# Kernel optimization log

Measured on AMD Instinct MI355X. Metric: run time of the kernel, lower is better.

The kernel has to match this reference:

```python
import jax, jax.numpy as jnp
import numpy as np

NHEADS = 16
KVHEADS = 4
HEAD_DIM = 128  # emb_kq_per_head == emb_v_per_head
ROPE_THETA = 10000.0


def _rotary(x, cos, sin):
    # x: [B, S, H, D]; half-split rotation
    x1, x2 = jnp.split(x, 2, axis=-1)
    rot = jnp.concatenate([-x2, x1], axis=-1)
    return x * cos + rot * sin


def setup_inputs() -> dict:
    key = jax.random.key(0)
    k1, k2, k3 = jax.random.split(key, 3)
    B, S, E = 2, 2048, 2048
    qkv_out = NHEADS * HEAD_DIM + 2 * KVHEADS * HEAD_DIM  # 3072
    return {
        "x": jax.random.normal(k1, (B, S, E), dtype=jnp.float32),
        "w_qkv": jax.random.normal(k2, (E, qkv_out), dtype=jnp.float32) * 0.02,
        "w_dense": jax.random.normal(k3, (NHEADS * HEAD_DIM, E), dtype=jnp.float32) * 0.02,
    }


def reference(x, w_qkv, w_dense):
    B, S, E = x.shape
    D = HEAD_DIM
    # fused QKV projection (use_bias=False), then split per FusedQKV.splits
    qkv = x @ w_qkv  # [B, S, 3072]
    q, k, v = jnp.split(qkv, [NHEADS * D, NHEADS * D + KVHEADS * D], axis=-1)
    q = q.reshape(B, S, NHEADS, D)
    k = k.reshape(B, S, KVHEADS, D)
    v = v.reshape(B, S, KVHEADS, D)

    # rotary position encoding, positions = arange(S)
    pos = jnp.arange(S, dtype=jnp.float32)
    inv_freq = 1.0 / (ROPE_THETA ** (jnp.arange(0, D, 2, dtype=jnp.float32) / D))
    ang = pos[:, None] * inv_freq[None, :]                 # [S, D/2]
    ang = jnp.concatenate([ang, ang], axis=-1)             # [S, D]
    cos = jnp.cos(ang)[None, :, None, :]                   # [1, S, 1, D]
    sin = jnp.sin(ang)[None, :, None, :]
    q = _rotary(q, cos, sin)
    k = _rotary(k, cos, sin)

    # GQA: expand kv heads to query heads
    rep = NHEADS // KVHEADS
    k = jnp.repeat(k, rep, axis=2)  # [B, S, NHEADS, D]
    v = jnp.repeat(v, rep, axis=2)

    scale = 1.0 / jnp.sqrt(jnp.asarray(D, dtype=x.dtype))
    scores = jnp.einsum("bqhd,bkhd->bhqk", q, k) * scale   # [B, H, S, S]
    causal = jnp.tril(jnp.ones((S, S), dtype=bool))
    scores = jnp.where(causal[None, None], scores, jnp.finfo(scores.dtype).min)
    probs = jax.nn.softmax(scores, axis=-1)
    attn = jnp.einsum("bhqk,bkhd->bqhd", probs, v)         # [B, S, H, D]
    attn = attn.reshape(B, S, NHEADS * D)
    return attn @ w_dense                                  # [B, S, E]
```

## Files before the change

kernel.cpp:

```cpp
#include <hip/hip_runtime.h>
#include <type_traits>


typedef __attribute__((ext_vector_type(8))) short short8;
typedef __attribute__((ext_vector_type(4))) float floatx4;
typedef __attribute__((ext_vector_type(4))) unsigned short ushort4v;
typedef __attribute__((ext_vector_type(4))) unsigned int uint4v;

constexpr int NH    = 16;
constexpr int NKV   = 4;
constexpr int HD    = 128;
constexpr int SEQ   = 2048;
constexpr int EMB   = 2048;
constexpr int NBATCH = 2;
constexpr int MROWS = NBATCH * SEQ;
constexpr int NQKV  = (NH + 2 * NKV) * HD;

__device__ __forceinline__ unsigned short f2b(float f) {
  union { float f; unsigned u; } v; v.f = f;
  unsigned u = v.u + 0x7FFFu + ((v.u >> 16) & 1u);
  return (unsigned short)(u >> 16);
}
__device__ __forceinline__ float b2f(unsigned short h) {
  union { unsigned u; float f; } v; v.u = (unsigned)h << 16;
  return v.f;
}

__device__ __forceinline__ void gload_lds16(const unsigned short* g,
                                            unsigned short* lds) {
  __builtin_amdgcn_global_load_lds(
      (const __attribute__((address_space(1))) unsigned int*)g,
      (__attribute__((address_space(3))) unsigned int*)lds, 16, 0, 0);
}

__global__ void cvt_f32_bf16(const float* __restrict__ in,
                             unsigned short* __restrict__ out, int n) {
  int i = (blockIdx.x * 256 + threadIdx.x) * 4;
  if (i + 3 < n) {
    floatx4 v = *(const floatx4*)(in + i);
    ushort4v o = { f2b(v[0]), f2b(v[1]), f2b(v[2]), f2b(v[3]) };
    *(ushort4v*)(out + i) = o;
  }
}

__global__ void rope_table(float* __restrict__ tab) {
  int idx = blockIdx.x * 256 + threadIdx.x;
  int j = idx & 63, s = idx >> 6;
  float e = -(float)j * (2.0f * 13.287712379549449f / 128.0f);
  float ang = (float)s * exp2f(e);
  float sn, c;
  sincosf(ang, &sn, &c);
  tab[idx * 2]     = c;
  tab[idx * 2 + 1] = sn;
}

__global__ void transpose_cvt_dual(const float* __restrict__ wqkv,
                                   unsigned short* __restrict__ oqkv,
                                   const float* __restrict__ wd,
                                   unsigned short* __restrict__ od) {
  const int z = blockIdx.z;
  const float* in = z ? wd : wqkv;
  unsigned short* out = z ? od : oqkv;
  const int R = EMB;
  const int C = z ? EMB : NQKV;
  int c0 = blockIdx.x * 32, r0 = blockIdx.y * 32;
  if (c0 >= C) return;
  __shared__ float t[32][33];
  int tx = threadIdx.x & 31, ty = threadIdx.x >> 5;
#pragma unroll
  for (int i = 0; i < 32; i += 8)
    t[ty + i][tx] = in[(long)(r0 + ty + i) * C + (c0 + tx)];
  __syncthreads();
#pragma unroll
  for (int i = 0; i < 32; i += 8)
    out[(long)(c0 + ty + i) * R + (r0 + tx)] = f2b(t[tx][ty + i]);
}

constexpr int BM = 128, BK = 64;

template <int MODE>
__global__ __launch_bounds__(256, MODE == 1 ? 4 : 3) void gemm_bt(
    const unsigned short* __restrict__ A,
    const unsigned short* __restrict__ BT,
    int Mdim, int Ndim, int Kdim,
    float* __restrict__ outF,
    unsigned short* __restrict__ Qb,
    unsigned short* __restrict__ Kb,
    unsigned short* __restrict__ Vt,
    const float* __restrict__ ropetab,
    float qscale) {
  constexpr int TBN = (MODE == 1) ? 64 : 128;
  constexpr int NI  = TBN / 32;
  __shared__ __align__(16) unsigned short smem[BM * BK + TBN * BK];
  unsigned short (*As)[BK] = (unsigned short (*)[BK])smem;
  unsigned short (*Bs)[BK] = (unsigned short (*)[BK])(smem + BM * BK);
  const int tid = threadIdx.x;
  const int bm = blockIdx.y * BM;
  const int bn = blockIdx.x * TBN;
  const int wave = tid >> 6, lane = tid & 63;
  const int l = lane & 15, q = lane >> 4;
  const int l7 = l & 7;
  const int wm = (wave >> 1) * 64, wn = (wave & 1) * (TBN / 2);

  floatx4 acc[4][NI] = {};

  const int srow = lane >> 3;
  const int scol = ((lane & 7) ^ srow) * 8;
  const unsigned short* Arow = A + (long)bm * Kdim;
  const unsigned short* Brow = BT + (long)bn * Kdim;

  for (int k0 = 0; k0 < Kdim; k0 += BK) {
#pragma unroll
    for (int i = 0; i < 4; ++i) {
      const int r0 = wave * 32 + i * 8;
      gload_lds16(Arow + (long)(r0 + srow) * Kdim + k0 + scol, &As[r0][0]);
    }
#pragma unroll
    for (int i = 0; i < TBN / 32; ++i) {
      const int r0 = wave * (TBN / 4) + i * 8;
      gload_lds16(Brow + (long)(r0 + srow) * Kdim + k0 + scol, &Bs[r0][0]);
    }
    __syncthreads();
#pragma unroll
    for (int kk = 0; kk < 2; ++kk) {
      short8 af[4], bfr[NI];
#pragma unroll
      for (int mi = 0; mi < 4; ++mi)
        af[mi] = *(const short8*)&As[wm + mi * 16 + l][((kk * 4 + q) ^ l7) * 8];
#pragma unroll
      for (int ni = 0; ni < NI; ++ni)
        bfr[ni] = *(const short8*)&Bs[wn + ni * 16 + l][((kk * 4 + q) ^ l7) * 8];
#pragma unroll
      for (int mi = 0; mi < 4; ++mi)
#pragma unroll
        for (int ni = 0; ni < NI; ++ni)
          acc[mi][ni] = __builtin_amdgcn_mfma_f32_16x16x32_bf16(
              af[mi], bfr[ni], acc[mi][ni], 0, 0, 0);
    }
    __syncthreads();
  }

  if constexpr (MODE == 1) {
#pragma unroll
    for (int mi = 0; mi < 4; ++mi) {
      const int rowbase = bm + wm + mi * 16 + q * 4;
#pragma unroll
      for (int ni = 0; ni < NI; ++ni) {
        const int col = bn + wn + ni * 16 + l;
#pragma unroll
        for (int r = 0; r < 4; ++r)
          outF[(long)(rowbase + r) * Ndim + col] = acc[mi][ni][r];
      }
    }
    return;
  }

  unsigned short (*Ct)[128] = (unsigned short (*)[128])smem;
#pragma unroll
  for (int mi = 0; mi < 4; ++mi)
#pragma unroll
    for (int ni = 0; ni < NI; ++ni)
#pragma unroll
      for (int r = 0; r < 4; ++r) {
        const int row = wm + mi * 16 + q * 4 + r;
        const int col = wn + ni * 16 + l;
        const int cs = ((((col >> 3) ^ row) & 7) | (col & 64 ? 8 : 0)) * 8 + (col & 7);
        Ct[row][cs] = f2b(acc[mi][ni][r]);
      }
  __syncthreads();

  if (bn >= (NH + NKV) * HD) {
    const int hh = (bn - (NH + NKV) * HD) >> 7;
    const int d = tid >> 1, ch = tid & 1;
    const int m0 = bm + ch * 64;
    const int bb = m0 >> 11, sbase = m0 & (SEQ - 1);
    unsigned short* vrow =
        Vt + ((long)(bb * NKV + hh)) * HD * SEQ + (long)d * SEQ + sbase;
    const int dblk = d >> 3, dlo = d & 7, dhi = (d & 64) ? 8 : 0;
#pragma unroll
    for (int pb = 0; pb < 8; ++pb) {
      short8 ov;
#pragma unroll
      for (int j = 0; j < 8; ++j) {
        const int p6 = pb * 8 + j;
        const int s6 = (p6 & 32) | ((p6 & 24) >> 1) | ((p6 & 4) << 2) | (p6 & 3);
        const int row = ch * 64 + s6;
        const int cs = (((dblk ^ row) & 7) | dhi) * 8 + dlo;
        ov[j] = (short)Ct[row][cs];
      }
      *(short8*)(vrow + pb * 8) = ov;
    }
  } else {
    const int row = tid >> 1, g = tid & 1;
    const int m = bm + row, bb = m >> 11, s = m & (SEQ - 1);
    const bool isQ = (bn < NH * HD);
    unsigned short* dst;
    if (isQ) dst = Qb + (((long)(bb * NH + (bn >> 7))) * SEQ + s) * HD;
    else     dst = Kb + (((long)(bb * NKV + ((bn - NH * HD) >> 7))) * SEQ + s) * HD;
    const float scale = isQ ? qscale : 1.0f;
    const float* trow = ropetab + (long)s * 128;
#pragma unroll
    for (int i = 0; i < 8; ++i) {
      const int lbo = g * 8 + i;
      const int lbx = (g ^ 1) * 8 + i;
      const int pbo = (lbo & 8) | ((lbo ^ row) & 7);
      const int pbx = (lbx & 8) | ((lbx ^ row) & 7);
      short8 xo = *(const short8*)&Ct[row][pbo * 8];
      short8 xx = *(const short8*)&Ct[row][pbx * 8];
      floatx4 t0 = *(const floatx4*)(trow + i * 16);
      floatx4 t1 = *(const floatx4*)(trow + i * 16 + 4);
      floatx4 t2 = *(const floatx4*)(trow + i * 16 + 8);
      floatx4 t3 = *(const floatx4*)(trow + i * 16 + 12);
      const float cc[8] = { t0[0], t0[2], t1[0], t1[2], t2[0], t2[2], t3[0], t3[2] };
      const float ss[8] = { t0[1], t0[3], t1[1], t1[3], t2[1], t2[3], t3[1], t3[3] };
      short8 outv;
#pragma unroll
      for (int j2 = 0; j2 < 8; ++j2) {
        const float xown = b2f((unsigned short)xo[j2]);
        const float xoth = b2f((unsigned short)xx[j2]);
        const float rr = g ? (xown * cc[j2] + xoth * ss[j2])
                           : (xown * cc[j2] - xoth * ss[j2]);
        outv[j2] = (short)f2b(rr * scale);
      }
      *(short8*)(dst + g * 64 + i * 8) = outv;
    }
  }
}

__global__ __launch_bounds__(256, 2) void attn_kernel(
    const unsigned short* __restrict__ Q,
    const unsigned short* __restrict__ K,
    const unsigned short* __restrict__ VT,
    unsigned short* __restrict__ attn) {
  const int h = blockIdx.y, b = blockIdx.z;
  const int t = b ? (15 - (int)blockIdx.x) : (int)blockIdx.x;
  const int kvh = h >> 2;
  const int tid = threadIdx.x;
  const int wave = tid >> 6, lane = tid & 63;
  const int l = lane & 15, q = lane >> 4;
  const int l7 = l & 7;
  const int wq = wave * 32;

  const unsigned short* Kh  = K  + ((long)(b * NKV + kvh)) * SEQ * HD;
  const unsigned short* VTh = VT + ((long)(b * NKV + kvh)) * HD * SEQ;

  __shared__ __align__(16) unsigned short smem[2 * 64 * 128 + 2 * 128 * 64];
  unsigned short (*Ks)[64 * 128]  = (unsigned short (*)[64 * 128])smem;
  unsigned short (*VTs)[128 * 64] = (unsigned short (*)[128 * 64])(smem + 2 * 64 * 128);

  int koff[4], voff[4];
  {
    const int k_rl = lane >> 4, k_bp = lane & 15;
    const int v_rl = lane >> 3, v_bp = lane & 7;
#pragma unroll
    for (int j = 0; j < 4; ++j) {
      const int rk = (wave * 4 + j) * 4 + k_rl;
      koff[j] = rk * HD + (k_bp ^ (rk & 15)) * 8;
      const int rv = (wave * 4 + j) * 8 + v_rl;
      voff[j] = rv * SEQ + (v_bp ^ (rv & 7)) * 8;
    }
  }

  short8 onesf;
#pragma unroll
  for (int i = 0; i < 8; ++i) onesf[i] = (short)0x3F80;

  auto stage = [&](int c, int buf) {
    const unsigned short* kc = Kh + c * (64 * HD);
    const unsigned short* vc = VTh + c * 64;
#pragma unroll
    for (int j = 0; j < 4; ++j)
      gload_lds16(kc + koff[j], &Ks[buf][(wave * 4 + j) * 4 * 128]);
#pragma unroll
    for (int j = 0; j < 4; ++j)
      gload_lds16(vc + voff[j], &VTs[buf][(wave * 4 + j) * 8 * 64]);
  };

  const unsigned short* Qh = Q + (((long)(b * NH + h)) * SEQ + t * 128) * HD;
  short8 qf[2][4];
#pragma unroll
  for (int mh = 0; mh < 2; ++mh)
#pragma unroll
    for (int kk = 0; kk < 4; ++kk)
      qf[mh][kk] = *(const short8*)(Qh + (long)(wq + mh * 16 + l) * HD + kk * 32 + q * 8);

  floatx4 o[2][9] = {};

  auto chunk_body = [&](auto masked, int cur, int kv0) {
    constexpr bool MASKED = decltype(masked)::value;
    floatx4 sf[2][4] = {};
#pragma unroll
    for (int kk = 0; kk < 4; ++kk) {
      short8 kf[4];
#pragma unroll
      for (int ni = 0; ni < 4; ++ni)
        kf[ni] = *(const short8*)&Ks[cur][(ni * 16 + l) * 128 + (((kk * 4 + q) ^ l) * 8)];
#pragma unroll
      for (int mh = 0; mh < 2; ++mh)
#pragma unroll
        for (int ni = 0; ni < 4; ++ni)
          sf[mh][ni] = __builtin_amdgcn_mfma_f32_16x16x32_bf16(
              kf[ni], qf[mh][kk], sf[mh][ni], 0, 0, 0);
    }
    short8 pf[2][2];
#pragma unroll
    for (int mh = 0; mh < 2; ++mh) {
      const int qrow = t * 128 + wq + mh * 16 + l;
      unsigned u[8];
#pragma unroll
      for (int ni = 0; ni < 4; ++ni) {
        if constexpr (MASKED) {
#pragma unroll
          for (int r = 0; r < 4; ++r)
            if (kv0 + ni * 16 + q * 4 + r > qrow) sf[mh][ni][r] = -3e38f;
        }
        float e0 = exp2f(sf[mh][ni][0]);
        float e1 = exp2f(sf[mh][ni][1]);
        float e2 = exp2f(sf[mh][ni][2]);
        float e3 = exp2f(sf[mh][ni][3]);
        asm("v_cvt_pk_bf16_f32 %0, %1, %2" : "=v"(u[ni * 2]) : "v"(e0), "v"(e1));
        asm("v_cvt_pk_bf16_f32 %0, %1, %2" : "=v"(u[ni * 2 + 1]) : "v"(e2), "v"(e3));
      }
      union { uint4v v; short8 s; } a0, a1;
      a0.v = (uint4v){u[0], u[1], u[2], u[3]};
      a1.v = (uint4v){u[4], u[5], u[6], u[7]};
      pf[mh][0] = a0.s;
      pf[mh][1] = a1.s;
    }
#pragma unroll
    for (int c2 = 0; c2 < 2; ++c2) {
      const int pb = ((c2 * 4 + q) ^ l7) * 8;
#pragma unroll
      for (int di = 0; di < 8; ++di) {
        short8 vf = *(const short8*)&VTs[cur][(di * 16 + l) * 64 + pb];
        o[0][di] = __builtin_amdgcn_mfma_f32_16x16x32_bf16(pf[0][c2], vf, o[0][di], 0, 0, 0);
        o[1][di] = __builtin_amdgcn_mfma_f32_16x16x32_bf16(pf[1][c2], vf, o[1][di], 0, 0, 0);
      }
      o[0][8] = __builtin_amdgcn_mfma_f32_16x16x32_bf16(pf[0][c2], onesf, o[0][8], 0, 0, 0);
      o[1][8] = __builtin_amdgcn_mfma_f32_16x16x32_bf16(pf[1][c2], onesf, o[1][8], 0, 0, 0);
    }
  };

  const int nc = 2 * t + 2;
  stage(0, 0);
  __syncthreads();

  int c = 0;
#pragma unroll 1
  for (; c < nc - 2; ++c) {
    stage(c + 1, (c & 1) ^ 1);
    chunk_body(std::false_type{}, c & 1, c * 64);
    __syncthreads();
  }
  stage(c + 1, (c & 1) ^ 1);
  chunk_body(std::true_type{}, c & 1, c * 64);
  __syncthreads();
  ++c;
  chunk_body(std::true_type{}, c & 1, c * 64);
  __syncthreads();

  unsigned short (*Ob)[136] = (unsigned short (*)[136])smem;
#pragma unroll
  for (int mh = 0; mh < 2; ++mh)
#pragma unroll
    for (int r = 0; r < 4; ++r) {
      const float inv = 1.0f / o[mh][8][r];
#pragma unroll
      for (int di = 0; di < 8; ++di)
        Ob[wq + mh * 16 + q * 4 + r][di * 16 + l] = f2b(o[mh][di][r] * inv);
    }
  __syncthreads();
  {
    const int row = tid >> 1, g = (tid & 1) * 64;
    const int s = t * 128 + row;
    unsigned short* dst = attn + ((long)(b * SEQ + s)) * (NH * HD) + h * HD + g;
#pragma unroll
    for (int j = 0; j < 8; ++j)
      *(short8*)(dst + j * 8) = *(const short8*)&Ob[row][g + j * 8];
  }
}

extern "C" void kernel_launch(void* const* d_in, const int* in_sizes, int n_in,
                              void* d_out, int out_size, void* d_ws, size_t ws_size,
                              hipStream_t stream) {
  const float* x       = (const float*)d_in[0];
  const float* w_qkv   = (const float*)d_in[1];
  const float* w_dense = (const float*)d_in[2];
  float* out = (float*)d_out;

  char* ws = (char*)d_ws;
  const size_t MB = 1024 * 1024;
  unsigned short* xb    = (unsigned short*)(ws);
  unsigned short* wqkvT = (unsigned short*)(ws + 16 * MB);
  unsigned short* wdT   = (unsigned short*)(ws + 28 * MB);
  unsigned short* Qb    = (unsigned short*)(ws + 36 * MB);
  unsigned short* Kb    = (unsigned short*)(ws + 52 * MB);
  unsigned short* VTb   = (unsigned short*)(ws + 56 * MB);
  float*          rtab  = (float*)(ws + 60 * MB);
  unsigned short* attn  = xb;

  const float qscale = 0.08838834764831845f * 1.4426950408889634f;

  rope_table<<<(SEQ * 64) / 256, 256, 0, stream>>>(rtab);
  cvt_f32_bf16<<<(MROWS * EMB) / (256 * 4), 256, 0, stream>>>(x, xb, MROWS * EMB);
  transpose_cvt_dual<<<dim3(NQKV / 32, EMB / 32, 2), 256, 0, stream>>>(
      w_qkv, wqkvT, w_dense, wdT);

  gemm_bt<0><<<dim3(NQKV / 128, MROWS / BM), 256, 0, stream>>>(
      xb, wqkvT, MROWS, NQKV, EMB, nullptr, Qb, Kb, VTb, rtab, qscale);

  attn_kernel<<<dim3(16, NH, NBATCH), 256, 0, stream>>>(Qb, Kb, VTb, attn);

  gemm_bt<1><<<dim3(EMB / 64, MROWS / BM), 256, 0, stream>>>(
      attn, wdT, MROWS, EMB, NH * HD, out, nullptr, nullptr, nullptr, nullptr, 0.0f);
}
```

Measured before the change: 275.3 us.

## Merge prep kernels, remap GEMM blocks across XCDs, raise MFMA priority in attention

Merges the three preprocessing launches (x conversion, weight transpose-convert, rope table) into one flat-grid prep kernel, removing two launches and the idle tail of the transpose grid. The GEMM block index is remapped so consecutive tiles land on the same XCD (stride-8 interleave), aiming for better L2 reuse of shared operand tiles. In attention, s_setprio brackets the MFMA sections so waves issuing matrix ops get scheduling priority over others. Each change is small and independent. The remap assumes the block count divides evenly by 8.

```diff
diff --git a/kernel.cpp b/kernel.cpp
--- a/kernel.cpp
+++ b/kernel.cpp
@@ -33,47 +33,54 @@
       (__attribute__((address_space(3))) unsigned int*)lds, 16, 0, 0);
 }
 
-__global__ void cvt_f32_bf16(const float* __restrict__ in,
-                             unsigned short* __restrict__ out, int n) {
-  int i = (blockIdx.x * 256 + threadIdx.x) * 4;
-  if (i + 3 < n) {
-    floatx4 v = *(const floatx4*)(in + i);
+constexpr int PREP_CVT   = 8192;
+constexpr int PREP_TQKV  = PREP_CVT + 6144;
+constexpr int PREP_TD    = PREP_TQKV + 4096;
+constexpr int PREP_TOTAL = PREP_TD + 512;
+
+__global__ __launch_bounds__(256) void prep(
+    const float* __restrict__ x, unsigned short* __restrict__ xb,
+    const float* __restrict__ wqkv, unsigned short* __restrict__ oqkv,
+    const float* __restrict__ wd, unsigned short* __restrict__ od,
+    float* __restrict__ rtab) {
+  const int blk = blockIdx.x;
+  const int tid = threadIdx.x;
+  __shared__ float t[32][33];
+  if (blk < PREP_CVT) {
+    const int i = (blk * 256 + tid) * 4;
+    floatx4 v = *(const floatx4*)(x + i);
     ushort4v o = { f2b(v[0]), f2b(v[1]), f2b(v[2]), f2b(v[3]) };
-    *(ushort4v*)(out + i) = o;
-  }
-}
-
-__global__ void rope_table(float* __restrict__ tab) {
-  int idx = blockIdx.x * 256 + threadIdx.x;
-  int j = idx & 63, s = idx >> 6;
-  float e = -(float)j * (2.0f * 13.287712379549449f / 128.0f);
-  float ang = (float)s * exp2f(e);
-  float sn, c;
-  sincosf(ang, &sn, &c);
-  tab[idx * 2]     = c;
-  tab[idx * 2 + 1] = sn;
-}
-
-__global__ void transpose_cvt_dual(const float* __restrict__ wqkv,
-                                   unsigned short* __restrict__ oqkv,
-                                   const float* __restrict__ wd,
-                                   unsigned short* __restrict__ od) {
-  const int z = blockIdx.z;
-  const float* in = z ? wd : wqkv;
-  unsigned short* out = z ? od : oqkv;
-  const int R = EMB;
-  const int C = z ? EMB : NQKV;
-  int c0 = blockIdx.x * 32, r0 = blockIdx.y * 32;
-  if (c0 >= C) return;
-  __shared__ float t[32][33];
-  int tx = threadIdx.x & 31, ty = threadIdx.x >> 5;
-#pragma unroll
-  for (int i = 0; i < 32; i += 8)
-    t[ty + i][tx] = in[(long)(r0 + ty + i) * C + (c0 + tx)];
-  __syncthreads();
-#pragma unroll
-  for (int i = 0; i < 32; i += 8)
-    out[(long)(c0 + ty + i) * R + (r0 + tx)] = f2b(t[tx][ty + i]);
+    *(ushort4v*)(xb + i) = o;
+  } else if (blk < PREP_TD) {
+    const float* in;
+    unsigned short* out;
+    int C, cx, ry;
+    if (blk < PREP_TQKV) {
+      const int local = blk - PREP_CVT;
+      in = wqkv; out = oqkv; C = NQKV; cx = local % 96; ry = local / 96;
+    } else {
+      const int local = blk - PREP_TQKV;
+      in = wd; out = od; C = EMB; cx = local % 64; ry = local / 64;
+    }
+    const int c0 = cx * 32, r0 = ry * 32;
+    const int tx = tid & 31, ty = tid >> 5;
+#pragma unroll
+    for (int i = 0; i < 32; i += 8)
+      t[ty + i][tx] = in[(long)(r0 + ty + i) * C + (c0 + tx)];
+    __syncthreads();
+#pragma unroll
+    for (int i = 0; i < 32; i += 8)
+      out[(long)(c0 + ty + i) * EMB + (r0 + tx)] = f2b(t[tx][ty + i]);
+  } else {
+    const int idx = (blk - PREP_TD) * 256 + tid;
+    const int j = idx & 63, s = idx >> 6;
+    const float e = -(float)j * (2.0f * 13.287712379549449f / 128.0f);
+    const float ang = (float)s * exp2f(e);
+    float sn, c;
+    sincosf(ang, &sn, &c);
+    rtab[idx * 2]     = c;
+    rtab[idx * 2 + 1] = sn;
+  }
 }
 
 constexpr int BM = 128, BK = 64;
@@ -95,8 +102,11 @@
   unsigned short (*As)[BK] = (unsigned short (*)[BK])smem;
   unsigned short (*Bs)[BK] = (unsigned short (*)[BK])(smem + BM * BK);
   const int tid = threadIdx.x;
-  const int bm = blockIdx.y * BM;
-  const int bn = blockIdx.x * TBN;
+  const int nwg = gridDim.x * gridDim.y;
+  const int orig = blockIdx.x + gridDim.x * blockIdx.y;
+  const int id = (orig & 7) * (nwg >> 3) + (orig >> 3);
+  const int bm = (id / gridDim.x) * BM;
+  const int bn = (id % gridDim.x) * TBN;
   const int wave = tid >> 6, lane = tid & 63;
   const int l = lane & 15, q = lane >> 4;
   const int l7 = l & 7;
@@ -295,12 +305,14 @@
 #pragma unroll
       for (int ni = 0; ni < 4; ++ni)
         kf[ni] = *(const short8*)&Ks[cur][(ni * 16 + l) * 128 + (((kk * 4 + q) ^ l) * 8)];
+      __builtin_amdgcn_s_setprio(1);
 #pragma unroll
       for (int mh = 0; mh < 2; ++mh)
 #pragma unroll
         for (int ni = 0; ni < 4; ++ni)
           sf[mh][ni] = __builtin_amdgcn_mfma_f32_16x16x32_bf16(
               kf[ni], qf[mh][kk], sf[mh][ni], 0, 0, 0);
+      __builtin_amdgcn_s_setprio(0);
     }
     short8 pf[2][2];
 #pragma unroll
@@ -330,6 +342,7 @@
 #pragma unroll
     for (int c2 = 0; c2 < 2; ++c2) {
       const int pb = ((c2 * 4 + q) ^ l7) * 8;
+      __builtin_amdgcn_s_setprio(1);
 #pragma unroll
       for (int di = 0; di < 8; ++di) {
         short8 vf = *(const short8*)&VTs[cur][(di * 16 + l) * 64 + pb];
@@ -338,6 +351,7 @@
       }
       o[0][8] = __builtin_amdgcn_mfma_f32_16x16x32_bf16(pf[0][c2], onesf, o[0][8], 0, 0, 0);
       o[1][8] = __builtin_amdgcn_mfma_f32_16x16x32_bf16(pf[1][c2], onesf, o[1][8], 0, 0, 0);
+      __builtin_amdgcn_s_setprio(0);
     }
   };
 
@@ -401,10 +415,7 @@
 
   const float qscale = 0.08838834764831845f * 1.4426950408889634f;
 
-  rope_table<<<(SEQ * 64) / 256, 256, 0, stream>>>(rtab);
-  cvt_f32_bf16<<<(MROWS * EMB) / (256 * 4), 256, 0, stream>>>(x, xb, MROWS * EMB);
-  transpose_cvt_dual<<<dim3(NQKV / 32, EMB / 32, 2), 256, 0, stream>>>(
-      w_qkv, wqkvT, w_dense, wdT);
+  prep<<<PREP_TOTAL, 256, 0, stream>>>(x, xb, w_qkv, wqkvT, w_dense, wdT, rtab);
 
   gemm_bt<0><<<dim3(NQKV / 128, MROWS / BM), 256, 0, stream>>>(
       xb, wqkvT, MROWS, NQKV, EMB, nullptr, Qb, Kb, VTb, rtab, qscale);
```

Result: slower. 285.7 us (+3.8%).
